# Kernel tuning notes

Hardware: AMD Instinct MI355X
Metric: run time of the kernel (lower is better)

## Reference

```python
import jax, jax.numpy as jnp
import numpy as np

INPUT_DIM = 1024
HIDDEN_DIM = 2048
NUM_EMB = 4096
EMB_DIM = 256
N = 65536


def setup_inputs() -> dict:
    key = jax.random.key(0)
    ks = jax.random.split(key, 10)
    s = lambda fan_in: 1.0 / np.sqrt(fan_in)
    return {
        "x": jax.random.normal(ks[0], (N, INPUT_DIM), dtype=jnp.float32),
        # encoder: Linear(input_dim, hidden) -> ReLU -> Linear(hidden, emb)
        "W1": jax.random.uniform(ks[1], (INPUT_DIM, HIDDEN_DIM), jnp.float32, -s(INPUT_DIM), s(INPUT_DIM)),
        "b1": jax.random.uniform(ks[2], (HIDDEN_DIM,), jnp.float32, -s(INPUT_DIM), s(INPUT_DIM)),
        "W2": jax.random.uniform(ks[3], (HIDDEN_DIM, EMB_DIM), jnp.float32, -s(HIDDEN_DIM), s(HIDDEN_DIM)),
        "b2": jax.random.uniform(ks[4], (EMB_DIM,), jnp.float32, -s(HIDDEN_DIM), s(HIDDEN_DIM)),
        # codebook (nn.Embedding weight)
        "codebook": jax.random.normal(ks[5], (NUM_EMB, EMB_DIM), dtype=jnp.float32),
        # decoder: Linear(emb, hidden) -> ReLU -> Linear(hidden, input_dim)
        "W3": jax.random.uniform(ks[6], (EMB_DIM, HIDDEN_DIM), jnp.float32, -s(EMB_DIM), s(EMB_DIM)),
        "b3": jax.random.uniform(ks[7], (HIDDEN_DIM,), jnp.float32, -s(EMB_DIM), s(EMB_DIM)),
        "W4": jax.random.uniform(ks[8], (HIDDEN_DIM, INPUT_DIM), jnp.float32, -s(HIDDEN_DIM), s(HIDDEN_DIM)),
        "b4": jax.random.uniform(ks[9], (INPUT_DIM,), jnp.float32, -s(HIDDEN_DIM), s(HIDDEN_DIM)),
    }


def reference(x, W1, b1, W2, b2, codebook, W3, b3, W4, b4):
    # encoder
    h = jax.nn.relu(x @ W1 + b1)
    encoded = h @ W2 + b2                      # [N, E]
    # cdist (squared form; argmin is identical to Euclidean argmin)
    enc_sq = jnp.sum(encoded * encoded, axis=-1, keepdims=True)   # [N, 1]
    cb_sq = jnp.sum(codebook * codebook, axis=-1)                 # [K]
    d2 = enc_sq - 2.0 * (encoded @ codebook.T) + cb_sq            # [N, K]
    indices = jnp.argmin(d2, axis=-1)                             # [N]
    quantized = codebook[indices]                                 # [N, E]
    # decoder
    h2 = jax.nn.relu(quantized @ W3 + b3)
    decoded = h2 @ W4 + b4
    return (quantized, decoded)
```

## Files before the change

### kernel.cpp

```cpp
#include <hip/hip_runtime.h>

#define N_ROWS 65536
#define IN_DIM 1024
#define HID    2048
#define EMB    256
#define NCODE  4096

typedef __attribute__((ext_vector_type(8))) short bf16x8;
typedef __attribute__((ext_vector_type(4))) float f32x4;

__device__ __forceinline__ unsigned short f2bf(float v) {
    unsigned u = __float_as_uint(v);
    u += 0x7FFFu + ((u >> 16) & 1u);
    return (unsigned short)(u >> 16);
}
__device__ __forceinline__ float bf2f(unsigned short h) {
    return __uint_as_float(((unsigned)h) << 16);
}
__device__ __forceinline__ void gload16(const unsigned short* g, unsigned short* l) {
    __builtin_amdgcn_global_load_lds(
        (const __attribute__((address_space(1))) unsigned int*)g,
        (__attribute__((address_space(3))) unsigned int*)l, 16, 0, 0);
}

template<int SPLIT>
__global__ __launch_bounds__(256) void k_conv_w(
    const float* __restrict__ src, unsigned short* __restrict__ dh,
    unsigned short* __restrict__ dl, int NC, int nkt)
{
    const int t = threadIdx.x;
    const int nt = blockIdx.x, kt = blockIdx.y;
    const int kk = t >> 2, j4 = (t & 3) << 2;
    const int k0 = kt << 6, n0 = nt << 4;
    float4 v = *(const float4*)(src + (size_t)(k0 + kk) * NC + n0 + j4);
    size_t tb = ((size_t)nt * nkt + kt) * 1024 + ((kk >> 3) * 128) + (kk & 7);
    float vv[4] = {v.x, v.y, v.z, v.w};
    #pragma unroll
    for (int j = 0; j < 4; ++j) {
        unsigned short h = f2bf(vv[j]);
        dh[tb + (size_t)(j4 + j) * 8] = h;
        if (SPLIT) dl[tb + (size_t)(j4 + j) * 8] = f2bf(vv[j] - bf2f(h));
    }
}

__global__ __launch_bounds__(256) void k_conv_a2(
    const float* __restrict__ src, unsigned short* __restrict__ dh,
    unsigned short* __restrict__ dl, int Kw, int nkt)
{
    const int t = threadIdx.x;
    const int mt = blockIdx.x, kt = blockIdx.y;
    const int rr = t >> 4, k4 = (t & 15) << 2;
    float4 v = *(const float4*)(src + (size_t)(mt * 16 + rr) * Kw + kt * 64 + k4);
    size_t addr = ((size_t)mt * nkt + kt) * 1024 + (k4 >> 3) * 128 + rr * 8 + (k4 & 7);
    ushort4 h = { f2bf(v.x), f2bf(v.y), f2bf(v.z), f2bf(v.w) };
    ushort4 lo = { f2bf(v.x - bf2f(h.x)), f2bf(v.y - bf2f(h.y)),
                   f2bf(v.z - bf2f(h.z)), f2bf(v.w - bf2f(h.w)) };
    *(ushort4*)&dh[addr] = h;
    *(ushort4*)&dl[addr] = lo;
}

__global__ __launch_bounds__(256) void k_conv_cb(
    const float* __restrict__ cb, unsigned short* __restrict__ ch,
    unsigned short* __restrict__ cl_, float* __restrict__ halfsq)
{
    const int t = threadIdx.x;
    const int ct = blockIdx.x;
    const int cl = t >> 4, f = t & 15;
    const int code = (ct << 4) + cl;
    float ssq = 0.f;
    #pragma unroll
    for (int it = 0; it < 4; ++it) {
        const int k4 = (f << 2) + (it << 6);
        float4 v = *(const float4*)(cb + (size_t)code * EMB + k4);
        ssq += v.x * v.x + v.y * v.y + v.z * v.z + v.w * v.w;
        size_t tb = ((size_t)(ct * 4 + (k4 >> 6))) * 1024 + ((k4 >> 3) & 7) * 128 + cl * 8 + (k4 & 7);
        ushort4 h = { f2bf(v.x), f2bf(v.y), f2bf(v.z), f2bf(v.w) };
        *(ushort4*)&ch[tb] = h;
        ushort4 lo = { f2bf(v.x - bf2f(h.x)), f2bf(v.y - bf2f(h.y)),
                       f2bf(v.z - bf2f(h.z)), f2bf(v.w - bf2f(h.w)) };
        *(ushort4*)&cl_[tb] = lo;
    }
    #pragma unroll
    for (int off = 1; off <= 8; off <<= 1) ssq += __shfl_xor(ssq, off);
    if (f == 0) halfsq[code] = 0.5f * ssq;
}

template<int SPLIT, int AFMT, int OUTT>
__global__ __launch_bounds__(512, 1) void k_layer2(
    const float* __restrict__ A, const unsigned short* __restrict__ At,
    const unsigned short* __restrict__ Atl, int a_nkt,
    int lda, int K,
    const unsigned short* __restrict__ Bh, const unsigned short* __restrict__ Bl,
    int b_nkt, const float* __restrict__ bias, int biasoff,
    float* __restrict__ out, unsigned short* __restrict__ outt,
    unsigned short* __restrict__ outt2,
    int outw, int relu, int init, int ny_log2)
{
    constexpr int BUFSZ = SPLIT ? 32768 : 24576;
    constexpr int AL = 8192;
    constexpr int BH = SPLIT ? 16384 : 8192;
    __shared__ __align__(16) unsigned short s_mem[2 * BUFSZ];

    const int t = threadIdx.x;
    const int id = blockIdx.x;
    const int m_low = id & 7, rest = id >> 3;
    const int nb = rest & ((1 << ny_log2) - 1);
    const int m0 = (((rest >> ny_log2) << 3) | m_low) * 128;
    const int nb0 = nb * 256;
    const int lane = t & 63, wv = t >> 6;
    const int wm = wv >> 2, wn = wv & 3;
    const int g = lane >> 4, rr = lane & 15;
    const int nt = K >> 6;

    f32x4 acc[4][4];
    #pragma unroll
    for (int mi = 0; mi < 4; ++mi)
        #pragma unroll
        for (int ni = 0; ni < 4; ++ni) acc[mi][ni] = (f32x4){0.f, 0.f, 0.f, 0.f};

    #define STAGE_DMA(buf, ktile)                                                      \
        {                                                                              \
            unsigned short* base_ = &s_mem[(buf) * BUFSZ];                             \
            _Pragma("unroll")                                                          \
            for (int jj = 0; jj < 2; ++jj) {                                           \
                const int j_ = wv * 2 + jj;                                            \
                const size_t gt_ = ((size_t)(nb0 / 16 + j_) * b_nkt + (ktile)) * 1024; \
                _Pragma("unroll")                                                      \
                for (int hf = 0; hf < 2; ++hf)                                         \
                    gload16(Bh + gt_ + hf * 512 + lane * 8,                            \
                            base_ + BH + j_ * 1024 + hf * 512);                        \
            }                                                                          \
            if (AFMT >= 1) {                                                           \
                const size_t ga_ = ((size_t)(m0 / 16 + wv) * a_nkt + (ktile)) * 1024;  \
                _Pragma("unroll")                                                      \
                for (int hf = 0; hf < 2; ++hf)                                         \
                    gload16(At + ga_ + hf * 512 + lane * 8,                            \
                            base_ + wv * 1024 + hf * 512);                             \
                if (AFMT == 2) {                                                       \
                    _Pragma("unroll")                                                  \
                    for (int hf = 0; hf < 2; ++hf)                                     \
                        gload16(Atl + ga_ + hf * 512 + lane * 8,                       \
                                base_ + AL + wv * 1024 + hf * 512);                    \
                }                                                                      \
            }                                                                          \
        }

    #define A_LOAD(ktile, pv)                                                          \
        {                                                                              \
            _Pragma("unroll")                                                          \
            for (int it = 0; it < 4; ++it) {                                           \
                int f_ = t + (it << 9);                                                \
                int r_ = f_ >> 4, k4_ = (f_ & 15) << 2;                                \
                pv[it] = *(const float4*)(A + (size_t)(m0 + r_) * lda + (ktile) * 64 + k4_); \
            }                                                                          \
        }

    #define A_WRITE(buf, pv)                                                           \
        {                                                                              \
            unsigned short* base_ = &s_mem[(buf) * BUFSZ];                             \
            _Pragma("unroll")                                                          \
            for (int it = 0; it < 4; ++it) {                                           \
                int f_ = t + (it << 9);                                                \
                int r_ = f_ >> 4, k4_ = (f_ & 15) << 2;                                \
                int mt_ = r_ >> 4, rl_ = r_ & 15, kb_ = k4_ >> 3, e_ = k4_ & 7;        \
                int addr_ = mt_ * 1024 + kb_ * 128 + ((rl_ ^ kb_) << 3) + e_;          \
                float4 v_ = pv[it];                                                    \
                ushort4 hi_, lo_;                                                      \
                hi_.x = f2bf(v_.x); hi_.y = f2bf(v_.y); hi_.z = f2bf(v_.z); hi_.w = f2bf(v_.w); \
                *(ushort4*)&base_[addr_] = hi_;                                        \
                if (SPLIT) {                                                           \
                    lo_.x = f2bf(v_.x - bf2f(hi_.x)); lo_.y = f2bf(v_.y - bf2f(hi_.y)); \
                    lo_.z = f2bf(v_.z - bf2f(hi_.z)); lo_.w = f2bf(v_.w - bf2f(hi_.w)); \
                    *(ushort4*)&base_[AL + addr_] = lo_;                               \
                }                                                                      \
            }                                                                          \
        }

    #define COMPUTE(buf, ktile)                                                        \
        {                                                                              \
            const unsigned short* base_ = &s_mem[(buf) * BUFSZ];                       \
            __builtin_amdgcn_s_setprio(1);                                             \
            _Pragma("unroll")                                                          \
            for (int s = 0; s < 2; ++s) {                                              \
                const int kb = (s << 2) + g;                                           \
                bf16x8 a_h[4], a_l[4], b_h[4], b_l[4];                                 \
                _Pragma("unroll")                                                      \
                for (int i = 0; i < 4; ++i) {                                          \
                    int arow = (AFMT == 0) ? (((rr ^ kb) & 15) << 3) : (rr << 3);      \
                    int aaddr = (wm * 4 + i) * 1024 + kb * 128 + arow;                 \
                    a_h[i] = *(const bf16x8*)&base_[aaddr];                            \
                    if (SPLIT) a_l[i] = *(const bf16x8*)&base_[AL + aaddr];            \
                    int baddr = (wn * 4 + i) * 1024 + kb * 128 + (rr << 3);            \
                    b_h[i] = *(const bf16x8*)&base_[BH + baddr];                       \
                    if (SPLIT)                                                         \
                        b_l[i] = *(const bf16x8*)(Bl +                                 \
                            ((size_t)(nb0 / 16 + wn * 4 + i) * b_nkt + (ktile)) * 1024 \
                            + kb * 128 + (rr << 3));                                   \
                }                                                                      \
                _Pragma("unroll")                                                      \
                for (int mi = 0; mi < 4; ++mi)                                         \
                    _Pragma("unroll")                                                  \
                    for (int ni = 0; ni < 4; ++ni) {                                   \
                        acc[mi][ni] = __builtin_amdgcn_mfma_f32_16x16x32_bf16(a_h[mi], b_h[ni], acc[mi][ni], 0, 0, 0); \
                        if (SPLIT) {                                                   \
                            acc[mi][ni] = __builtin_amdgcn_mfma_f32_16x16x32_bf16(a_l[mi], b_h[ni], acc[mi][ni], 0, 0, 0); \
                            acc[mi][ni] = __builtin_amdgcn_mfma_f32_16x16x32_bf16(a_h[mi], b_l[ni], acc[mi][ni], 0, 0, 0); \
                        }                                                              \
                    }                                                                  \
            }                                                                          \
            __builtin_amdgcn_s_setprio(0);                                             \
        }

    float4 pv[4];
    STAGE_DMA(0, 0)
    if (AFMT == 0) {
        A_LOAD(0, pv)
        A_WRITE(0, pv)
    }
    asm volatile("s_waitcnt vmcnt(0) lgkmcnt(0)" ::: "memory");
    __builtin_amdgcn_s_barrier();
    __builtin_amdgcn_sched_barrier(0);

    int cur = 0;
    for (int kt = 0; kt < nt; ++kt) {
        if (kt + 1 < nt) {
            STAGE_DMA(cur ^ 1, kt + 1)
            if (AFMT == 0) A_LOAD(kt + 1, pv)
        }
        COMPUTE(cur, kt)
        if (AFMT == 0) { if (kt + 1 < nt) A_WRITE(cur ^ 1, pv) }
        asm volatile("s_waitcnt vmcnt(0) lgkmcnt(0)" ::: "memory");
        __builtin_amdgcn_s_barrier();
        __builtin_amdgcn_sched_barrier(0);
        cur ^= 1;
    }
    #undef STAGE_DMA
    #undef A_LOAD
    #undef A_WRITE
    #undef COMPUTE

    if (OUTT == 0) {
        float* sf = (float*)s_mem;
        for (int rm = 0; rm < 2; ++rm) {
            if (wm == rm) {
                #pragma unroll
                for (int mi = 0; mi < 4; ++mi)
                    #pragma unroll
                    for (int ni = 0; ni < 4; ++ni)
                        #pragma unroll
                        for (int rg = 0; rg < 4; ++rg)
                            sf[(mi * 16 + g * 4 + rg) * 256 + wn * 64 + ni * 16 + rr] = acc[mi][ni][rg];
            }
            __syncthreads();
            #pragma unroll
            for (int it = 0; it < 8; ++it) {
                int f = t + (it << 9);
                int r = f >> 6, c4 = (f & 63) << 2;
                float4 v = *(const float4*)&sf[r * 256 + c4];
                int gr = m0 + rm * 64 + r, gc = nb0 + c4;
                float* op = out + (size_t)gr * outw + gc;
                if (init) {
                    v.x += bias[biasoff + gc + 0]; v.y += bias[biasoff + gc + 1];
                    v.z += bias[biasoff + gc + 2]; v.w += bias[biasoff + gc + 3];
                } else {
                    float4 o = *(const float4*)op;
                    v.x += o.x; v.y += o.y; v.z += o.z; v.w += o.w;
                }
                if (relu) {
                    v.x = fmaxf(v.x, 0.f); v.y = fmaxf(v.y, 0.f);
                    v.z = fmaxf(v.z, 0.f); v.w = fmaxf(v.w, 0.f);
                }
                *(float4*)op = v;
            }
            __syncthreads();
        }
    } else {
        const int npass = (OUTT == 2) ? 2 : 1;
        for (int pass = 0; pass < npass; ++pass) {
            #pragma unroll
            for (int mi = 0; mi < 4; ++mi)
                #pragma unroll
                for (int ni = 0; ni < 4; ++ni) {
                    const int c = wn * 64 + ni * 16 + rr;
                    float bb = bias[biasoff + nb0 + c];
                    #pragma unroll
                    for (int rg = 0; rg < 4; ++rg) {
                        float v = acc[mi][ni][rg] + bb;
                        if (relu) v = fmaxf(v, 0.f);
                        unsigned short hi = f2bf(v);
                        unsigned short w = (pass == 0) ? hi : f2bf(v - bf2f(hi));
                        int addr = ((wm * 4 + mi) * 4 + wn) * 1024
                                 + (ni * 2 + (rr >> 3)) * 128 + (g * 4 + rg) * 8 + (rr & 7);
                        s_mem[addr] = w;
                    }
                }
            __syncthreads();
            unsigned short* dst = (pass == 0) ? outt : outt2;
            #pragma unroll
            for (int it = 0; it < 8; ++it) {
                int f = t + (it << 9);
                int tl = f >> 7, w8 = f & 127;
                size_t gaddr = ((size_t)(m0 / 16 + (tl >> 2)) * outw + nb0 / 64 + (tl & 3)) * 1024;
                *(float4*)(dst + gaddr + w8 * 8) = *(const float4*)&s_mem[tl * 1024 + w8 * 8];
            }
            __syncthreads();
        }
    }
}

__global__ __launch_bounds__(512, 2) void k_dist(
    float* encq, const unsigned short* __restrict__ ch,
    const unsigned short* __restrict__ cl,
    const float* __restrict__ hsq, const float* __restrict__ cb,
    unsigned short* __restrict__ qt)
{
    __shared__ __align__(16) unsigned short s_cb[2][16384];
    __shared__ int s_c1[256], s_c2[256];

    const int t = threadIdx.x;
    const int lane = t & 63, wv = t >> 6;
    const int g = lane >> 4, rr = lane & 15;
    const int r0 = blockIdx.x * 256;

    bf16x8 eh[2][8], el[2][8];
    #pragma unroll
    for (int rg = 0; rg < 2; ++rg) {
        const float* ep = encq + (size_t)(r0 + wv * 32 + rg * 16 + rr) * EMB + g * 8;
        #pragma unroll
        for (int s = 0; s < 8; ++s) {
            float4 v0 = *(const float4*)(ep + s * 32);
            float4 v1 = *(const float4*)(ep + s * 32 + 4);
            float vv[8] = {v0.x, v0.y, v0.z, v0.w, v1.x, v1.y, v1.z, v1.w};
            bf16x8 a, b;
            #pragma unroll
            for (int j = 0; j < 8; ++j) {
                unsigned short h = f2bf(vv[j]);
                a[j] = (short)h;
                b[j] = (short)f2bf(vv[j] - bf2f(h));
            }
            eh[rg][s] = a; el[rg][s] = b;
        }
    }
    float b1v[2][4], b2v[2][4]; int i1v[2][4], i2v[2][4];
    #pragma unroll
    for (int rg = 0; rg < 2; ++rg)
        #pragma unroll
        for (int r2 = 0; r2 < 4; ++r2) {
            b1v[rg][r2] = -1e30f; b2v[rg][r2] = -1e30f;
            i1v[rg][r2] = 0; i2v[rg][r2] = 0;
        }

    #define STAGE(buf, c)                                                              \
        {                                                                              \
            const unsigned short* gh_ = ch + (size_t)(c) * 8192 + wv * 1024;           \
            const unsigned short* gl_ = cl + (size_t)(c) * 8192 + wv * 1024;           \
            _Pragma("unroll")                                                          \
            for (int i_ = 0; i_ < 2; ++i_) {                                           \
                gload16(gh_ + i_ * 512 + lane * 8, &s_cb[buf][wv * 1024 + i_ * 512]);  \
                gload16(gl_ + i_ * 512 + lane * 8, &s_cb[buf][8192 + wv * 1024 + i_ * 512]); \
            }                                                                          \
        }

    #define COMPUTE(cur, c, hv_)                                                       \
        {                                                                              \
            f32x4 ahh[2][2], ahl[2][2], alh[2][2];                                     \
            _Pragma("unroll")                                                          \
            for (int rg = 0; rg < 2; ++rg)                                             \
                _Pragma("unroll")                                                      \
                for (int ci = 0; ci < 2; ++ci) {                                       \
                    ahh[rg][ci] = (f32x4){0.f, 0.f, 0.f, 0.f};                         \
                    ahl[rg][ci] = (f32x4){0.f, 0.f, 0.f, 0.f};                         \
                    alh[rg][ci] = (f32x4){0.f, 0.f, 0.f, 0.f};                         \
                }                                                                      \
            __builtin_amdgcn_s_setprio(1);                                             \
            _Pragma("unroll")                                                          \
            for (int s = 0; s < 8; ++s) {                                              \
                const int ktile = s >> 1, kb = ((s & 1) << 2) + g;                     \
                _Pragma("unroll")                                                      \
                for (int ci = 0; ci < 2; ++ci) {                                       \
                    const int off = (ci * 4 + ktile) * 1024 + kb * 128 + rr * 8;       \
                    bf16x8 bh = *(const bf16x8*)&s_cb[cur][off];                       \
                    bf16x8 bl = *(const bf16x8*)&s_cb[cur][8192 + off];                \
                    _Pragma("unroll")                                                  \
                    for (int rg = 0; rg < 2; ++rg) {                                   \
                        ahh[rg][ci] = __builtin_amdgcn_mfma_f32_16x16x32_bf16(eh[rg][s], bh, ahh[rg][ci], 0, 0, 0); \
                        ahl[rg][ci] = __builtin_amdgcn_mfma_f32_16x16x32_bf16(eh[rg][s], bl, ahl[rg][ci], 0, 0, 0); \
                        alh[rg][ci] = __builtin_amdgcn_mfma_f32_16x16x32_bf16(el[rg][s], bh, alh[rg][ci], 0, 0, 0); \
                    }                                                                  \
                }                                                                      \
            }                                                                          \
            __builtin_amdgcn_s_setprio(0);                                             \
            _Pragma("unroll")                                                          \
            for (int rg = 0; rg < 2; ++rg)                                             \
                _Pragma("unroll")                                                      \
                for (int ci = 0; ci < 2; ++ci) {                                       \
                    f32x4 av = ahh[rg][ci] + ahl[rg][ci] + alh[rg][ci];                \
                    const int code = ((c) << 5) + (ci << 4) + rr;                      \
                    const float hs = __shfl(hv_, ci * 16 + rr);                        \
                    _Pragma("unroll")                                                  \
                    for (int r2 = 0; r2 < 4; ++r2) {                                   \
                        float v = av[r2] - hs;                                         \
                        bool bt1 = (v > b1v[rg][r2]) || (v == b1v[rg][r2] && code < i1v[rg][r2]); \
                        bool bt2 = (v > b2v[rg][r2]) || (v == b2v[rg][r2] && code < i2v[rg][r2]); \
                        if (bt1) { b2v[rg][r2] = b1v[rg][r2]; i2v[rg][r2] = i1v[rg][r2]; \
                                   b1v[rg][r2] = v; i1v[rg][r2] = code; }              \
                        else if (bt2) { b2v[rg][r2] = v; i2v[rg][r2] = code; }         \
                    }                                                                  \
                }                                                                      \
        }

    STAGE(0, 0)
    int cur = 0;
    for (int c = 0; c < 127; ++c) {
        STAGE(cur ^ 1, c + 1)
        float hv_ = hsq[(c << 5) + (lane & 31)];
        asm volatile("s_waitcnt vmcnt(5)" ::: "memory");
        __builtin_amdgcn_s_barrier();
        __builtin_amdgcn_sched_barrier(0);
        COMPUTE(cur, c, hv_)
        asm volatile("" ::: "memory");
        __builtin_amdgcn_s_barrier();
        cur ^= 1;
    }
    {
        float hv_ = hsq[(127 << 5) + (lane & 31)];
        asm volatile("s_waitcnt vmcnt(0)" ::: "memory");
        __builtin_amdgcn_s_barrier();
        __builtin_amdgcn_sched_barrier(0);
        COMPUTE(cur, 127, hv_)
    }
    #undef STAGE
    #undef COMPUTE

    #pragma unroll
    for (int off = 1; off <= 8; off <<= 1) {
        #pragma unroll
        for (int rg = 0; rg < 2; ++rg)
            #pragma unroll
            for (int r2 = 0; r2 < 4; ++r2) {
                float ob1 = __shfl_xor(b1v[rg][r2], off), ob2 = __shfl_xor(b2v[rg][r2], off);
                int oi1 = __shfl_xor(i1v[rg][r2], off), oi2 = __shfl_xor(i2v[rg][r2], off);
                bool ofirst = (ob1 > b1v[rg][r2]) || (ob1 == b1v[rg][r2] && oi1 < i1v[rg][r2]);
                if (ofirst) {
                    bool mysec = (b1v[rg][r2] > ob2) || (b1v[rg][r2] == ob2 && i1v[rg][r2] < oi2);
                    b2v[rg][r2] = mysec ? b1v[rg][r2] : ob2; i2v[rg][r2] = mysec ? i1v[rg][r2] : oi2;
                    b1v[rg][r2] = ob1; i1v[rg][r2] = oi1;
                } else {
                    bool osec = (ob1 > b2v[rg][r2]) || (ob1 == b2v[rg][r2] && oi1 < i2v[rg][r2]);
                    b2v[rg][r2] = osec ? ob1 : b2v[rg][r2]; i2v[rg][r2] = osec ? oi1 : i2v[rg][r2];
                }
            }
    }
    if (rr == 0) {
        #pragma unroll
        for (int rg = 0; rg < 2; ++rg)
            #pragma unroll
            for (int r2 = 0; r2 < 4; ++r2) {
                int rl = wv * 32 + rg * 16 + g * 4 + r2;
                s_c1[rl] = i1v[rg][r2]; s_c2[rl] = i2v[rg][r2];
            }
    }
    __syncthreads();

    for (int rloc = 0; rloc < 32; ++rloc) {
        const int row = wv * 32 + rloc;
        const int c1 = s_c1[row], c2 = s_c2[row];
        float4 ev = *(const float4*)(encq + (size_t)(r0 + row) * EMB + lane * 4);
        float4 v1 = *(const float4*)(cb + (size_t)c1 * EMB + lane * 4);
        float4 v2 = *(const float4*)(cb + (size_t)c2 * EMB + lane * 4);
        float d1 = ev.x * v1.x + ev.y * v1.y + ev.z * v1.z + ev.w * v1.w;
        float d2 = ev.x * v2.x + ev.y * v2.y + ev.z * v2.z + ev.w * v2.w;
        #pragma unroll
        for (int off = 1; off <= 32; off <<= 1) {
            d1 += __shfl_xor(d1, off);
            d2 += __shfl_xor(d2, off);
        }
        if (lane == 0) {
            float s1 = d1 - hsq[c1], s2 = d2 - hsq[c2];
            bool keep1 = (s1 > s2) || (s1 == s2 && c1 < c2);
            s_c1[row] = keep1 ? c1 : c2;
        }
    }
    __syncthreads();
    #pragma unroll
    for (int it = 0; it < 32; ++it) {
        int f = t + (it << 9);
        int row = f >> 6, c4 = (f & 63) << 2;
        int bi = s_c1[row];
        float4 qv = *(const float4*)(cb + (size_t)bi * EMB + c4);
        const int R = r0 + row;
        *(float4*)(encq + (size_t)R * EMB + c4) = qv;
        const int k4 = c4 & 63;
        size_t qaddr = ((size_t)(R >> 4) * 4 + (c4 >> 6)) * 1024
                     + (k4 >> 3) * 128 + (R & 15) * 8 + (k4 & 7);
        ushort4 qh = { f2bf(qv.x), f2bf(qv.y), f2bf(qv.z), f2bf(qv.w) };
        *(ushort4*)&qt[qaddr] = qh;
    }
}

__global__ __launch_bounds__(256) void k_dec_fb(
    const float* __restrict__ qz,
    const float* __restrict__ W3, const float* __restrict__ b3,
    const float* __restrict__ W4, const float* __restrict__ b4,
    float* __restrict__ outd) {
    __shared__ float s_q[8][EMB];
    __shared__ float s_h2[8][HID];
    const int t = threadIdx.x;
    const int row0 = blockIdx.x * 8;
    #pragma unroll
    for (int r = 0; r < 8; ++r) s_q[r][t] = qz[(size_t)(row0 + r) * EMB + t];
    __syncthreads();
    for (int gg = 0; gg < 8; ++gg) {
        const int j = (gg << 8) + t;
        float acc[8];
        #pragma unroll
        for (int r = 0; r < 8; ++r) acc[r] = 0.f;
        const float* wp = W3 + j;
        for (int e = 0; e < EMB; e += 4) {
            const float w0 = wp[(size_t)(e + 0) * HID];
            const float w1v = wp[(size_t)(e + 1) * HID];
            const float w2v = wp[(size_t)(e + 2) * HID];
            const float w3v = wp[(size_t)(e + 3) * HID];
            #pragma unroll
            for (int r = 0; r < 8; ++r) {
                const float4 qv = *reinterpret_cast<const float4*>(&s_q[r][e]);
                acc[r] = fmaf(qv.x, w0, acc[r]);
                acc[r] = fmaf(qv.y, w1v, acc[r]);
                acc[r] = fmaf(qv.z, w2v, acc[r]);
                acc[r] = fmaf(qv.w, w3v, acc[r]);
            }
        }
        const float bb = b3[j];
        #pragma unroll
        for (int r = 0; r < 8; ++r) s_h2[r][j] = fmaxf(acc[r] + bb, 0.f);
    }
    __syncthreads();
    float acc4[8][4];
    #pragma unroll
    for (int r = 0; r < 8; ++r)
        #pragma unroll
        for (int ci = 0; ci < 4; ++ci) acc4[r][ci] = 0.f;
    const float* w4p = W4 + t;
    for (int k = 0; k < HID; k += 4) {
        float wv[4][4];
        #pragma unroll
        for (int ki = 0; ki < 4; ++ki)
            #pragma unroll
            for (int ci = 0; ci < 4; ++ci)
                wv[ki][ci] = w4p[(size_t)(k + ki) * IN_DIM + (ci << 8)];
        #pragma unroll
        for (int r = 0; r < 8; ++r) {
            const float4 hv = *reinterpret_cast<const float4*>(&s_h2[r][k]);
            #pragma unroll
            for (int ci = 0; ci < 4; ++ci) {
                acc4[r][ci] = fmaf(hv.x, wv[0][ci], acc4[r][ci]);
                acc4[r][ci] = fmaf(hv.y, wv[1][ci], acc4[r][ci]);
                acc4[r][ci] = fmaf(hv.z, wv[2][ci], acc4[r][ci]);
                acc4[r][ci] = fmaf(hv.w, wv[3][ci], acc4[r][ci]);
            }
        }
    }
    #pragma unroll
    for (int ci = 0; ci < 4; ++ci) {
        const float bb = b4[(ci << 8) + t];
        #pragma unroll
        for (int r = 0; r < 8; ++r)
            outd[(size_t)(row0 + r) * IN_DIM + (ci << 8) + t] = acc4[r][ci] + bb;
    }
}

extern "C" void kernel_launch(void* const* d_in, const int* in_sizes, int n_in,
                              void* d_out, int out_size, void* d_ws, size_t ws_size,
                              hipStream_t stream) {
    const float* x  = (const float*)d_in[0];
    const float* W1 = (const float*)d_in[1];
    const float* b1 = (const float*)d_in[2];
    const float* W2 = (const float*)d_in[3];
    const float* b2 = (const float*)d_in[4];
    const float* cb = (const float*)d_in[5];
    const float* W3 = (const float*)d_in[6];
    const float* b3 = (const float*)d_in[7];
    const float* W4 = (const float*)d_in[8];
    const float* b4 = (const float*)d_in[9];

    float* outq = (float*)d_out;
    float* outd = outq + (size_t)N_ROWS * EMB;

    unsigned short* ou = (unsigned short*)outd;
    unsigned short* W1Th = ou;
    unsigned short* W1Tl = ou + 2097152;
    unsigned short* W2Th = ou + 4194304;
    unsigned short* W2Tl = ou + 4718592;
    unsigned short* cbh  = ou + 5242880;
    unsigned short* cbl  = ou + 6291456;
    float* halfsq = outd + 3670016;
    unsigned short* h_hi = (unsigned short*)(outd + 4194304);
    unsigned short* h_lo = h_hi + 33554432;
    unsigned short* qt = (unsigned short*)(outd + 58720256);
    float* enc = outq;

    const bool fastdec = ws_size >= (size_t)72351744;
    unsigned short* W3Th = (unsigned short*)d_ws;
    unsigned short* W4Th = W3Th + 524288;
    unsigned short* h2t  = (unsigned short*)((char*)d_ws + 5242880);
    unsigned short* xt_hi = h2t;
    unsigned short* xt_lo = h2t + 16777216;

    k_conv_w<1><<<dim3(128, 16), 256, 0, stream>>>(W1, W1Th, W1Tl, HID, 16);
    k_conv_w<1><<<dim3(16, 32), 256, 0, stream>>>(W2, W2Th, W2Tl, EMB, 32);
    k_conv_cb<<<256, 256, 0, stream>>>(cb, cbh, cbl, halfsq);
    if (fastdec) {
        k_conv_w<0><<<dim3(128, 4), 256, 0, stream>>>(W3, W3Th, nullptr, HID, 4);
        k_conv_w<0><<<dim3(64, 32), 256, 0, stream>>>(W4, W4Th, nullptr, IN_DIM, 32);
    }
    if (fastdec) {
        for (int s = 0; s < 4; ++s) {
            k_conv_a2<<<dim3(1024, 16), 256, 0, stream>>>(
                x + (size_t)s * 16777216, xt_hi, xt_lo, IN_DIM, 16);
            k_layer2<1, 2, 2><<<1024, 512, 0, stream>>>(
                nullptr, xt_hi, xt_lo, 16, 0, IN_DIM,
                W1Th, W1Tl, 16, b1, 0,
                nullptr, h_hi, h_lo, 32, 1, 0, 3);
            k_layer2<1, 2, 0><<<128, 512, 0, stream>>>(
                nullptr, h_hi, h_lo, 32, 0, HID,
                W2Th, W2Tl, 32, b2, 0,
                enc + (size_t)s * 4194304, nullptr, nullptr, EMB, 0, 1, 0);
        }
    } else {
        for (int q = 0; q < 4; ++q) {
            k_layer2<1, 0, 2><<<1024, 512, 0, stream>>>(
                x, nullptr, nullptr, 0, IN_DIM, IN_DIM,
                W1Th + (size_t)q * 524288, W1Tl + (size_t)q * 524288, 16,
                b1, q * 512, nullptr, h_hi, h_lo, 8, 1, 0, 1);
            k_layer2<1, 2, 0><<<512, 512, 0, stream>>>(
                nullptr, h_hi, h_lo, 8, 0, 512,
                W2Th + (size_t)q * 8192, W2Tl + (size_t)q * 8192, 32,
                b2, 0, enc, nullptr, nullptr, EMB, 0, q == 0, 0);
        }
    }
    k_dist<<<256, 512, 0, stream>>>(enc, cbh, cbl, halfsq, cb, qt);
    if (fastdec) {
        for (int s = 0; s < 4; ++s) {
            const size_t roff = (size_t)s * 16384;
            k_layer2<0, 1, 1><<<1024, 512, 0, stream>>>(
                nullptr, qt + (size_t)s * 4194304, nullptr, 4, 0, EMB,
                W3Th, nullptr, 4,
                b3, 0, nullptr, h2t, nullptr, 32, 1, 0, 3);
            k_layer2<0, 1, 0><<<512, 512, 0, stream>>>(
                nullptr, h2t, nullptr, 32, 0, HID,
                W4Th, nullptr, 32,
                b4, 0, outd + roff * IN_DIM, nullptr, nullptr, IN_DIM, 0, 1, 2);
        }
    } else {
        k_dec_fb<<<N_ROWS / 8, 256, 0, stream>>>(outq, W3, b3, W4, b4, outd);
    }
}
```

Baseline: 2.354 ms.

## Add dedicated layer-1 GEMM kernel with smaller tiles and two blocks per CU

Replaces the generic k_layer2 call for the first encoder GEMM with a specialized k_gemm1 kernel using 128x128 tiles, a 2048-block grid and launch_bounds(512,2), so two workgroups can share a CU. Only the high bf16 halves of A and B are staged through LDS with double buffering. The low halves are read straight from global memory inside the compute loop, which cuts LDS footprint but adds uncached-latency global loads on the MFMA path. The epilogue writes hi/lo bf16 outputs through LDS in two passes.

```diff
diff --git a/kernel.cpp b/kernel.cpp
--- a/kernel.cpp
+++ b/kernel.cpp
@@ -83,6 +83,131 @@
     #pragma unroll
     for (int off = 1; off <= 8; off <<= 1) ssq += __shfl_xor(ssq, off);
     if (f == 0) halfsq[code] = 0.5f * ssq;
+}
+
+__global__ __launch_bounds__(512, 2) void k_gemm1(
+    const unsigned short* __restrict__ At, const unsigned short* __restrict__ Atl,
+    int a_nkt,
+    const unsigned short* __restrict__ Bh, const unsigned short* __restrict__ Bl,
+    int b_nkt, int K,
+    const float* __restrict__ bias,
+    unsigned short* __restrict__ outt, unsigned short* __restrict__ outt2,
+    int out_nkt)
+{
+    constexpr int BUFSZ = 16384;
+    __shared__ __align__(16) unsigned short s_mem[2 * BUFSZ];
+
+    const int t = threadIdx.x;
+    const int id = blockIdx.x;
+    const int m_low = id & 7, rest = id >> 3;
+    const int nb = rest & 15;
+    const int m0 = (((rest >> 4) << 3) | m_low) * 128;
+    const int nb0 = nb * 128;
+    const int lane = t & 63, wv = t >> 6;
+    const int wm = wv >> 2, wn = wv & 3;
+    const int g = lane >> 4, rr = lane & 15;
+    const int nt = K >> 6;
+
+    f32x4 acc[4][2];
+    #pragma unroll
+    for (int mi = 0; mi < 4; ++mi)
+        #pragma unroll
+        for (int ni = 0; ni < 2; ++ni) acc[mi][ni] = (f32x4){0.f, 0.f, 0.f, 0.f};
+
+    #define G1_STAGE(buf, ktile)                                                       \
+        {                                                                              \
+            unsigned short* base_ = &s_mem[(buf) * BUFSZ];                             \
+            const size_t ga_ = ((size_t)(m0 / 16 + wv) * a_nkt + (ktile)) * 1024;      \
+            const size_t gb_ = ((size_t)((nb0 >> 4) + wv) * b_nkt + (ktile)) * 1024;   \
+            _Pragma("unroll")                                                          \
+            for (int hf = 0; hf < 2; ++hf) {                                           \
+                gload16(At + ga_ + hf * 512 + lane * 8, base_ + wv * 1024 + hf * 512); \
+                gload16(Bh + gb_ + hf * 512 + lane * 8, base_ + 8192 + wv * 1024 + hf * 512); \
+            }                                                                          \
+        }
+
+    #define G1_COMPUTE(buf, ktile)                                                     \
+        {                                                                              \
+            const unsigned short* base_ = &s_mem[(buf) * BUFSZ];                       \
+            __builtin_amdgcn_s_setprio(1);                                             \
+            _Pragma("unroll")                                                          \
+            for (int s = 0; s < 2; ++s) {                                              \
+                const int kb = (s << 2) + g;                                           \
+                bf16x8 a_h[4], a_l[4], b_h[2], b_l[2];                                 \
+                _Pragma("unroll")                                                      \
+                for (int i = 0; i < 4; ++i) {                                          \
+                    int aaddr = (wm * 4 + i) * 1024 + kb * 128 + (rr << 3);            \
+                    a_h[i] = *(const bf16x8*)&base_[aaddr];                            \
+                    a_l[i] = *(const bf16x8*)(Atl +                                    \
+                        ((size_t)(m0 / 16 + wm * 4 + i) * a_nkt + (ktile)) * 1024      \
+                        + kb * 128 + (rr << 3));                                       \
+                }                                                                      \
+                _Pragma("unroll")                                                      \
+                for (int j = 0; j < 2; ++j) {                                          \
+                    int baddr = 8192 + (wn * 2 + j) * 1024 + kb * 128 + (rr << 3);     \
+                    b_h[j] = *(const bf16x8*)&base_[baddr];                            \
+                    b_l[j] = *(const bf16x8*)(Bl +                                     \
+                        ((size_t)((nb0 >> 4) + wn * 2 + j) * b_nkt + (ktile)) * 1024   \
+                        + kb * 128 + (rr << 3));                                       \
+                }                                                                      \
+                _Pragma("unroll")                                                      \
+                for (int mi = 0; mi < 4; ++mi)                                         \
+                    _Pragma("unroll")                                                  \
+                    for (int ni = 0; ni < 2; ++ni) {                                   \
+                        acc[mi][ni] = __builtin_amdgcn_mfma_f32_16x16x32_bf16(a_h[mi], b_h[ni], acc[mi][ni], 0, 0, 0); \
+                        acc[mi][ni] = __builtin_amdgcn_mfma_f32_16x16x32_bf16(a_l[mi], b_h[ni], acc[mi][ni], 0, 0, 0); \
+                        acc[mi][ni] = __builtin_amdgcn_mfma_f32_16x16x32_bf16(a_h[mi], b_l[ni], acc[mi][ni], 0, 0, 0); \
+                    }                                                                  \
+            }                                                                          \
+            __builtin_amdgcn_s_setprio(0);                                             \
+        }
+
+    G1_STAGE(0, 0)
+    asm volatile("s_waitcnt vmcnt(0)" ::: "memory");
+    __builtin_amdgcn_s_barrier();
+    __builtin_amdgcn_sched_barrier(0);
+
+    int cur = 0;
+    for (int kt = 0; kt < nt; ++kt) {
+        if (kt + 1 < nt) G1_STAGE(cur ^ 1, kt + 1)
+        G1_COMPUTE(cur, kt)
+        asm volatile("s_waitcnt vmcnt(0)" ::: "memory");
+        __builtin_amdgcn_s_barrier();
+        __builtin_amdgcn_sched_barrier(0);
+        cur ^= 1;
+    }
+    #undef G1_STAGE
+    #undef G1_COMPUTE
+
+    for (int pass = 0; pass < 2; ++pass) {
+        #pragma unroll
+        for (int mi = 0; mi < 4; ++mi)
+            #pragma unroll
+            for (int ni = 0; ni < 2; ++ni) {
+                const int c = wn * 32 + ni * 16 + rr;
+                float bb = bias[nb0 + c];
+                const int ktl = c >> 6, k = c & 63;
+                #pragma unroll
+                for (int rg = 0; rg < 4; ++rg) {
+                    float v = fmaxf(acc[mi][ni][rg] + bb, 0.f);
+                    unsigned short hi = f2bf(v);
+                    unsigned short w = (pass == 0) ? hi : f2bf(v - bf2f(hi));
+                    int addr = ((wm * 4 + mi) * 2 + ktl) * 1024
+                             + ((k >> 3) & 7) * 128 + (g * 4 + rg) * 8 + (k & 7);
+                    s_mem[addr] = w;
+                }
+            }
+        __syncthreads();
+        unsigned short* dst = (pass == 0) ? outt : outt2;
+        #pragma unroll
+        for (int it = 0; it < 4; ++it) {
+            int f = t + (it << 9);
+            int tl = f >> 7, w8 = f & 127;
+            size_t gaddr = ((size_t)(m0 / 16 + (tl >> 1)) * out_nkt + (nb0 >> 6) + (tl & 1)) * 1024;
+            *(float4*)(dst + gaddr + w8 * 8) = *(const float4*)&s_mem[tl * 1024 + w8 * 8];
+        }
+        __syncthreads();
+    }
 }
 
 template<int SPLIT, int AFMT, int OUTT>
@@ -617,10 +742,8 @@
         for (int s = 0; s < 4; ++s) {
             k_conv_a2<<<dim3(1024, 16), 256, 0, stream>>>(
                 x + (size_t)s * 16777216, xt_hi, xt_lo, IN_DIM, 16);
-            k_layer2<1, 2, 2><<<1024, 512, 0, stream>>>(
-                nullptr, xt_hi, xt_lo, 16, 0, IN_DIM,
-                W1Th, W1Tl, 16, b1, 0,
-                nullptr, h_hi, h_lo, 32, 1, 0, 3);
+            k_gemm1<<<2048, 512, 0, stream>>>(
+                xt_hi, xt_lo, 16, W1Th, W1Tl, 16, IN_DIM, b1, h_hi, h_lo, 32);
             k_layer2<1, 2, 0><<<128, 512, 0, stream>>>(
                 nullptr, h_hi, h_lo, 32, 0, HID,
                 W2Th, W2Tl, 32, b2, 0,
```

Measured after the change: 2.356 ms. About the same (+0.1%).
